# Performance work log

Measured on AMD Instinct MI355X. Metric: run time of the kernel, lower is better.

## Reference

```python
import jax, jax.numpy as jnp
import numpy as np

B, C, H, W = 32, 32, 64, 64   # batch, in_channel, image height/width
HC = 1                        # hashtable channel groups (in_channel % HC == 0)
KS = 9                        # kernel_size: top-k neighbors per pixel
K = 64                        # kernel_number_per_pixel (output channels)
P = H * W                     # pixel_number


def setup_inputs() -> dict:
    key = jax.random.key(0)
    k1, k2, k3 = jax.random.split(key, 3)
    x = jax.random.normal(k1, (B, C, H, W), dtype=jnp.float32)
    # Per-pixel affinity scores -> top-KS neighbor indices (mimics
    # _build_full_hash: argsort descending, take first kernel_size).
    scores = jax.random.normal(k2, (HC, H, W, P), dtype=jnp.float32)
    idx = jnp.argsort(-scores, axis=-1)[..., :KS].astype(jnp.int32)  # (HC, NH, NW, KS)
    bound = float(np.sqrt(1.0 / (C * KS)))
    weights = jax.random.uniform(k3, (K, C * KS), minval=-bound, maxval=bound,
                                 dtype=jnp.float32)
    return {"x": x, "weights": weights, "idx": idx}


def reference(x, weights, idx):
    Bx, Cx, Hx, Wx = x.shape
    HCx, NH, NW, ks = idx.shape
    Px = Hx * Wx
    # full_hash[b, c, i, j, k] = idx[c % HC, i, j, k] + c*P + b*C*P,
    # so x.take(full_hash) == gather of x[b, c] at idx[c % HC].
    idx_full = jnp.tile(idx, (Cx // HCx, 1, 1, 1)).reshape(Cx, NH * NW * ks)
    g = jnp.take_along_axis(x.reshape(Bx, Cx, Px), idx_full[None], axis=2)  # (B, C, NH*NW*ks)
    # permute(1,4,0,2,3).reshape(C*ks, B*NH*NW)
    g = g.reshape(Bx, Cx, NH, NW, ks).transpose(1, 4, 0, 2, 3).reshape(Cx * ks, Bx * NH * NW)
    out = (weights @ g).reshape(-1, Bx, NH, NW)  # (K, B, NH, NW)
    return jnp.transpose(out, (1, 0, 2, 3))       # (B, K, NH, NW)
```

## Files before the change

### kernel.cpp

```cpp
#include <hip/hip_runtime.h>
#include <hip/hip_bf16.h>

#define BB 32
#define CC 32
#define PP 4096
#define KS 9
#define KK 64
#define CK 288

typedef __attribute__((ext_vector_type(8))) short short8;
typedef __attribute__((ext_vector_type(16))) float f32x16;

__device__ inline unsigned short f2bf(float f) {
    __hip_bfloat16 h = __float2bfloat16(f);
    return __builtin_bit_cast(unsigned short, h);
}

__global__ __launch_bounds__(256)
void prep_kernel(const float* __restrict__ x, const float* __restrict__ w,
                 unsigned short* __restrict__ xt, unsigned short* __restrict__ wa) {
    const int t = threadIdx.x;
    const int blk = blockIdx.x;
    if (blk < 512) {
        const int b = blk >> 4;
        const int p = ((blk & 15) << 8) + t;
        const float* xb = x + (size_t)b * CC * PP + p;
        unsigned int buf[16];
#pragma unroll
        for (int c2 = 0; c2 < 16; ++c2) {
            float lo = xb[(size_t)(2 * c2) * PP];
            float hi = xb[(size_t)(2 * c2 + 1) * PP];
            buf[c2] = (unsigned int)f2bf(lo) | ((unsigned int)f2bf(hi) << 16);
        }
        uint4* dst = (uint4*)(xt + ((size_t)b * PP + p) * CC);
        const uint4* s = (const uint4*)buf;
#pragma unroll
        for (int j = 0; j < 4; ++j) dst[j] = s[j];
    } else {
        int i = (blk - 512) * 256 + t;
        if (i < KK * CK) {
            int j  = i & 7;
            int l  = (i >> 3) & 63;
            int mt = (i >> 9) & 1;
            int kh = (i >> 10) & 1;
            int kc = i >> 11;
            int ko = (mt << 5) + (l & 31);
            int c  = (kh << 4) + ((l >> 5) << 3) + j;
            wa[i] = f2bf(w[ko * CK + c * KS + kc]);
        }
    }
}

__global__ __launch_bounds__(256, 4)
void abc_mfma5_kernel(const unsigned short* __restrict__ xt,
                      const unsigned short* __restrict__ wa,
                      const int* __restrict__ idx,
                      float* __restrict__ out) {
    __shared__ unsigned short was[KK * CK];
    const int t    = threadIdx.x;
    const int l    = t & 63;
    const int w    = t >> 6;
    const int blk  = blockIdx.x;
    const int b    = ((blk & 7) << 2) | ((blk >> 3) & 3);
    const int tile = blk >> 5;
    const int p0   = (tile << 7) + (w << 5);
    const int gpix  = l & 31;
    const int ghalf = l >> 5;

    {
        const uint4* s = (const uint4*)wa;
        uint4* d = (uint4*)was;
#pragma unroll
        for (int j = 0; j < 9; ++j) d[t + 256 * j] = s[t + 256 * j];
    }

    const unsigned short* xtb = xt + (size_t)b * PP * CC;

    int q[KS];
    {
        const int* ip = idx + (size_t)(p0 + gpix) * KS;
#pragma unroll
        for (int kc = 0; kc < KS; ++kc) q[kc] = ip[kc];
    }

    f32x16 acc[2];
#pragma unroll
    for (int i = 0; i < 16; ++i) { acc[0][i] = 0.f; acc[1][i] = 0.f; }

    __syncthreads();

    short8 g[3][2];
#pragma unroll
    for (int kk = 0; kk < 2; ++kk)
#pragma unroll
        for (int kh = 0; kh < 2; ++kh)
            g[kk][kh] = *(const short8*)(xtb + (size_t)q[kk] * CC + (kh << 4) + (ghalf << 3));

#pragma unroll
    for (int kc = 0; kc < KS; ++kc) {
        if (kc + 2 < KS) {
            const int nb = (kc + 2) % 3;
#pragma unroll
            for (int kh = 0; kh < 2; ++kh)
                g[nb][kh] = *(const short8*)(xtb + (size_t)q[kc + 2] * CC + (kh << 4) + (ghalf << 3));
        }
        const int cb = kc % 3;
#pragma unroll
        for (int mt = 0; mt < 2; ++mt) {
#pragma unroll
            for (int kh = 0; kh < 2; ++kh) {
                const short8 a =
                    *(const short8*)(was + ((size_t)(((kc * 2 + kh) * 2 + mt) * 64 + l)) * 8);
                acc[mt] = __builtin_amdgcn_mfma_f32_32x32x16_bf16(a, g[cb][kh], acc[mt], 0, 0, 0);
            }
        }
    }

    float* ob = out + (size_t)b * KK * PP + p0 + gpix;
#pragma unroll
    for (int mt = 0; mt < 2; ++mt)
#pragma unroll
        for (int r = 0; r < 16; ++r) {
            const int row = (mt << 5) + (r & 3) + ((r >> 2) << 3) + (ghalf << 2);
            __builtin_nontemporal_store(acc[mt][r], ob + (size_t)row * PP);
        }
}

__global__ __launch_bounds__(256)
void abc_valu_kernel(const float* __restrict__ x, const float* __restrict__ w,
                     const int* __restrict__ idx, float* __restrict__ out) {
    __shared__ float xrow[PP];
    const int t = threadIdx.x;
    const int b = blockIdx.x >> 4;
    const int p = ((blockIdx.x & 15) << 8) + t;
    int q[KS];
#pragma unroll
    for (int k = 0; k < KS; ++k) q[k] = idx[p * KS + k];
    float acc[KK];
#pragma unroll
    for (int i = 0; i < KK; ++i) acc[i] = 0.0f;
    const float* xb = x + (size_t)b * CC * PP;
#pragma unroll 1
    for (int c = 0; c < CC; ++c) {
        const float4* src = (const float4*)(xb + (size_t)c * PP);
        float4* dst = (float4*)xrow;
#pragma unroll
        for (int j = 0; j < 4; ++j) dst[j * 256 + t] = src[j * 256 + t];
        __syncthreads();
        float xv[KS];
#pragma unroll
        for (int k = 0; k < KS; ++k) xv[k] = xrow[q[k]];
#pragma unroll
        for (int k = 0; k < KS; ++k) {
            const int col = c * KS + k;
#pragma unroll
            for (int ko = 0; ko < KK; ++ko)
                acc[ko] += xv[k] * w[ko * CK + col];
        }
        __syncthreads();
    }
    float* ob = out + (size_t)b * KK * PP + p;
#pragma unroll
    for (int ko = 0; ko < KK; ++ko)
        ob[(size_t)ko * PP] = acc[ko];
}

extern "C" void kernel_launch(void* const* d_in, const int* in_sizes, int n_in,
                              void* d_out, int out_size, void* d_ws, size_t ws_size,
                              hipStream_t stream) {
    const float* x  = (const float*)d_in[0];
    const float* w  = (const float*)d_in[1];
    const int* idx  = (const int*)d_in[2];
    float* out      = (float*)d_out;

    const size_t xt_bytes = (size_t)BB * PP * CC * 2;
    const size_t need     = xt_bytes + (size_t)KK * CK * 2;

    if (ws_size >= need) {
        unsigned short* xt = (unsigned short*)d_ws;
        unsigned short* wa = (unsigned short*)((char*)d_ws + xt_bytes);
        const int wb_blocks = (KK * CK + 255) / 256;
        prep_kernel<<<512 + wb_blocks, 256, 0, stream>>>(x, w, xt, wa);
        abc_mfma5_kernel<<<BB * (PP / 128), 256, 0, stream>>>(xt, wa, idx, out);
    } else {
        abc_valu_kernel<<<BB * (PP / 256), 256, 0, stream>>>(x, w, idx, out);
    }
}
```

Before: 88.57 us.

## Fuse bf16 conversion and gather-GEMM into one kernel with LDS-resident image

Replaces the two-kernel pipeline (prep into a channel-last bf16 workspace, then MFMA gather) with one 1024-thread kernel. Each block stages half the channels of a whole image as packed bf16 in LDS, builds the weight fragments in LDS, and gathers neighbors from LDS instead of global memory. This removes the workspace round trip and one launch. In exchange each image is read and weights re-converted by 8 blocks, the grid drops to 256 large blocks with a big LDS footprint (about 150 KB), and the fallback VALU path is removed.

Result: no change. 86.98 us (-1.8%).

```diff
diff --git a/kernel.cpp b/kernel.cpp
--- a/kernel.cpp
+++ b/kernel.cpp
@@ -9,6 +9,7 @@
 #define CK 288
 
 typedef __attribute__((ext_vector_type(8))) short short8;
+typedef __attribute__((ext_vector_type(4))) int int4v;
 typedef __attribute__((ext_vector_type(16))) float f32x16;
 
 __device__ inline unsigned short f2bf(float f) {
@@ -16,65 +17,21 @@
     return __builtin_bit_cast(unsigned short, h);
 }
 
-__global__ __launch_bounds__(256)
-void prep_kernel(const float* __restrict__ x, const float* __restrict__ w,
-                 unsigned short* __restrict__ xt, unsigned short* __restrict__ wa) {
-    const int t = threadIdx.x;
-    const int blk = blockIdx.x;
-    if (blk < 512) {
-        const int b = blk >> 4;
-        const int p = ((blk & 15) << 8) + t;
-        const float* xb = x + (size_t)b * CC * PP + p;
-        unsigned int buf[16];
-#pragma unroll
-        for (int c2 = 0; c2 < 16; ++c2) {
-            float lo = xb[(size_t)(2 * c2) * PP];
-            float hi = xb[(size_t)(2 * c2 + 1) * PP];
-            buf[c2] = (unsigned int)f2bf(lo) | ((unsigned int)f2bf(hi) << 16);
-        }
-        uint4* dst = (uint4*)(xt + ((size_t)b * PP + p) * CC);
-        const uint4* s = (const uint4*)buf;
-#pragma unroll
-        for (int j = 0; j < 4; ++j) dst[j] = s[j];
-    } else {
-        int i = (blk - 512) * 256 + t;
-        if (i < KK * CK) {
-            int j  = i & 7;
-            int l  = (i >> 3) & 63;
-            int mt = (i >> 9) & 1;
-            int kh = (i >> 10) & 1;
-            int kc = i >> 11;
-            int ko = (mt << 5) + (l & 31);
-            int c  = (kh << 4) + ((l >> 5) << 3) + j;
-            wa[i] = f2bf(w[ko * CK + c * KS + kc]);
-        }
-    }
-}
+__global__ __launch_bounds__(1024)
+void abc_fused_kernel(const float* __restrict__ x, const float* __restrict__ w,
+                      const int* __restrict__ idx, float* __restrict__ out) {
+    __shared__ unsigned int   xs4[8 * 4100];
+    __shared__ unsigned short wah[9 * 2 * 64 * 8];
 
-__global__ __launch_bounds__(256, 4)
-void abc_mfma5_kernel(const unsigned short* __restrict__ xt,
-                      const unsigned short* __restrict__ wa,
-                      const int* __restrict__ idx,
-                      float* __restrict__ out) {
-    __shared__ unsigned short was[KK * CK];
-    const int t    = threadIdx.x;
-    const int l    = t & 63;
-    const int w    = t >> 6;
-    const int blk  = blockIdx.x;
-    const int b    = ((blk & 7) << 2) | ((blk >> 3) & 3);
-    const int tile = blk >> 5;
-    const int p0   = (tile << 7) + (w << 5);
+    const int t     = threadIdx.x;
+    const int l     = t & 63;
+    const int wv    = t >> 6;
+    const int blk   = blockIdx.x;
+    const int b     = ((blk & 7) << 2) | ((blk >> 3) & 3);
+    const int pb    = blk >> 5;
+    const int p0    = pb * 512 + wv * 32;
     const int gpix  = l & 31;
     const int ghalf = l >> 5;
-
-    {
-        const uint4* s = (const uint4*)wa;
-        uint4* d = (uint4*)was;
-#pragma unroll
-        for (int j = 0; j < 9; ++j) d[t + 256 * j] = s[t + 256 * j];
-    }
-
-    const unsigned short* xtb = xt + (size_t)b * PP * CC;
 
     int q[KS];
     {
@@ -87,31 +44,50 @@
 #pragma unroll
     for (int i = 0; i < 16; ++i) { acc[0][i] = 0.f; acc[1][i] = 0.f; }
 
-    __syncthreads();
-
-    short8 g[3][2];
-#pragma unroll
-    for (int kk = 0; kk < 2; ++kk)
-#pragma unroll
-        for (int kh = 0; kh < 2; ++kh)
-            g[kk][kh] = *(const short8*)(xtb + (size_t)q[kk] * CC + (kh << 4) + (ghalf << 3));
+    const float* xb0 = x + (size_t)b * CC * PP;
 
 #pragma unroll
-    for (int kc = 0; kc < KS; ++kc) {
-        if (kc + 2 < KS) {
-            const int nb = (kc + 2) % 3;
+    for (int half = 0; half < 2; ++half) {
+        if (half) __syncthreads();
+
+        const float* xh = xb0 + (size_t)(half * 16) * PP;
 #pragma unroll
-            for (int kh = 0; kh < 2; ++kh)
-                g[nb][kh] = *(const short8*)(xtb + (size_t)q[kc + 2] * CC + (kh << 4) + (ghalf << 3));
+        for (int c2 = 0; c2 < 8; ++c2) {
+            const float4 lo = *(const float4*)(xh + (size_t)(2 * c2) * PP + 4 * t);
+            const float4 hi = *(const float4*)(xh + (size_t)(2 * c2 + 1) * PP + 4 * t);
+            uint4 v;
+            v.x = (unsigned)f2bf(lo.x) | ((unsigned)f2bf(hi.x) << 16);
+            v.y = (unsigned)f2bf(lo.y) | ((unsigned)f2bf(hi.y) << 16);
+            v.z = (unsigned)f2bf(lo.z) | ((unsigned)f2bf(hi.z) << 16);
+            v.w = (unsigned)f2bf(lo.w) | ((unsigned)f2bf(hi.w) << 16);
+            *(uint4*)(&xs4[c2 * 4100 + 4 * t]) = v;
         }
-        const int cb = kc % 3;
+
 #pragma unroll
-        for (int mt = 0; mt < 2; ++mt) {
+        for (int i = 0; i < 9; ++i) {
+            const int wi = t + (i << 10);
+            const int j  = wi & 7;
+            const int ll = (wi >> 3) & 63;
+            const int mt = (wi >> 9) & 1;
+            const int kc = wi >> 10;
+            const int ko = (mt << 5) + (ll & 31);
+            const int c  = (half << 4) + ((ll >> 5) << 3) + j;
+            wah[wi] = f2bf(w[ko * CK + c * KS + kc]);
+        }
+
+        __syncthreads();
+
 #pragma unroll
-            for (int kh = 0; kh < 2; ++kh) {
-                const short8 a =
-                    *(const short8*)(was + ((size_t)(((kc * 2 + kh) * 2 + mt) * 64 + l)) * 8);
-                acc[mt] = __builtin_amdgcn_mfma_f32_32x32x16_bf16(a, g[cb][kh], acc[mt], 0, 0, 0);
+        for (int kc = 0; kc < KS; ++kc) {
+            int4v r;
+#pragma unroll
+            for (int jj = 0; jj < 4; ++jj)
+                r[jj] = (int)xs4[(ghalf * 4 + jj) * 4100 + q[kc]];
+            const short8 bf = __builtin_bit_cast(short8, r);
+#pragma unroll
+            for (int mt = 0; mt < 2; ++mt) {
+                const short8 a = *(const short8*)&wah[(((kc << 1) + mt) * 64 + l) * 8];
+                acc[mt] = __builtin_amdgcn_mfma_f32_32x32x16_bf16(a, bf, acc[mt], 0, 0, 0);
             }
         }
     }
@@ -126,45 +102,6 @@
         }
 }
 
-__global__ __launch_bounds__(256)
-void abc_valu_kernel(const float* __restrict__ x, const float* __restrict__ w,
-                     const int* __restrict__ idx, float* __restrict__ out) {
-    __shared__ float xrow[PP];
-    const int t = threadIdx.x;
-    const int b = blockIdx.x >> 4;
-    const int p = ((blockIdx.x & 15) << 8) + t;
-    int q[KS];
-#pragma unroll
-    for (int k = 0; k < KS; ++k) q[k] = idx[p * KS + k];
-    float acc[KK];
-#pragma unroll
-    for (int i = 0; i < KK; ++i) acc[i] = 0.0f;
-    const float* xb = x + (size_t)b * CC * PP;
-#pragma unroll 1
-    for (int c = 0; c < CC; ++c) {
-        const float4* src = (const float4*)(xb + (size_t)c * PP);
-        float4* dst = (float4*)xrow;
-#pragma unroll
-        for (int j = 0; j < 4; ++j) dst[j * 256 + t] = src[j * 256 + t];
-        __syncthreads();
-        float xv[KS];
-#pragma unroll
-        for (int k = 0; k < KS; ++k) xv[k] = xrow[q[k]];
-#pragma unroll
-        for (int k = 0; k < KS; ++k) {
-            const int col = c * KS + k;
-#pragma unroll
-            for (int ko = 0; ko < KK; ++ko)
-                acc[ko] += xv[k] * w[ko * CK + col];
-        }
-        __syncthreads();
-    }
-    float* ob = out + (size_t)b * KK * PP + p;
-#pragma unroll
-    for (int ko = 0; ko < KK; ++ko)
-        ob[(size_t)ko * PP] = acc[ko];
-}
-
 extern "C" void kernel_launch(void* const* d_in, const int* in_sizes, int n_in,
                               void* d_out, int out_size, void* d_ws, size_t ws_size,
                               hipStream_t stream) {
@@ -172,17 +109,7 @@
     const float* w  = (const float*)d_in[1];
     const int* idx  = (const int*)d_in[2];
     float* out      = (float*)d_out;
+    (void)d_ws; (void)ws_size;
 
-    const size_t xt_bytes = (size_t)BB * PP * CC * 2;
-    const size_t need     = xt_bytes + (size_t)KK * CK * 2;
-
-    if (ws_size >= need) {
-        unsigned short* xt = (unsigned short*)d_ws;
-        unsigned short* wa = (unsigned short*)((char*)d_ws + xt_bytes);
-        const int wb_blocks = (KK * CK + 255) / 256;
-        prep_kernel<<<512 + wb_blocks, 256, 0, stream>>>(x, w, xt, wa);
-        abc_mfma5_kernel<<<BB * (PP / 128), 256, 0, stream>>>(xt, wa, idx, out);
-    } else {
-        abc_valu_kernel<<<BB * (PP / 256), 256, 0, stream>>>(x, w, idx, out);
-    }
+    abc_fused_kernel<<<256, 1024, 0, stream>>>(x, w, idx, out);
 }
```

## Fuse bf16 conversion of x into MFMA kernel with LDS-staged channel groups

Applied to the files above, without the earlier changes.

Drops the separate prep pass that wrote a transposed bf16 copy of x to global memory. Each 1024-thread block now loads 8 channels of one image at a time, converts them to bf16 and stages them in double-buffered padded LDS. The neighbor gather then comes from LDS instead of scattered global reads. Weights are streamed per channel group in a new 4-wide packing, and the loads for the next group are prefetched while the MFMAs run. The cost is only 256 blocks with large LDS use (low occupancy), two barriers per group, and each block re-reading x for its pixel range.

New measurement: 92.49 us. 4.4% more time.

```diff
diff --git a/kernel.cpp b/kernel.cpp
--- a/kernel.cpp
+++ b/kernel.cpp
@@ -7,74 +7,51 @@
 #define KS 9
 #define KK 64
 #define CK 288
+#define PADP 4100
 
 typedef __attribute__((ext_vector_type(8))) short short8;
+typedef __attribute__((ext_vector_type(4))) float f32x4;
+typedef __attribute__((ext_vector_type(4))) int int4v;
+typedef __attribute__((ext_vector_type(2))) unsigned int u32x2;
+typedef __attribute__((ext_vector_type(4))) unsigned int u32x4;
 typedef __attribute__((ext_vector_type(16))) float f32x16;
 
-__device__ inline unsigned short f2bf(float f) {
+__device__ inline unsigned int f2bf(float f) {
     __hip_bfloat16 h = __float2bfloat16(f);
-    return __builtin_bit_cast(unsigned short, h);
+    return (unsigned int)__builtin_bit_cast(unsigned short, h);
 }
 
 __global__ __launch_bounds__(256)
-void prep_kernel(const float* __restrict__ x, const float* __restrict__ w,
-                 unsigned short* __restrict__ xt, unsigned short* __restrict__ wa) {
-    const int t = threadIdx.x;
-    const int blk = blockIdx.x;
-    if (blk < 512) {
-        const int b = blk >> 4;
-        const int p = ((blk & 15) << 8) + t;
-        const float* xb = x + (size_t)b * CC * PP + p;
-        unsigned int buf[16];
-#pragma unroll
-        for (int c2 = 0; c2 < 16; ++c2) {
-            float lo = xb[(size_t)(2 * c2) * PP];
-            float hi = xb[(size_t)(2 * c2 + 1) * PP];
-            buf[c2] = (unsigned int)f2bf(lo) | ((unsigned int)f2bf(hi) << 16);
-        }
-        uint4* dst = (uint4*)(xt + ((size_t)b * PP + p) * CC);
-        const uint4* s = (const uint4*)buf;
-#pragma unroll
-        for (int j = 0; j < 4; ++j) dst[j] = s[j];
-    } else {
-        int i = (blk - 512) * 256 + t;
-        if (i < KK * CK) {
-            int j  = i & 7;
-            int l  = (i >> 3) & 63;
-            int mt = (i >> 9) & 1;
-            int kh = (i >> 10) & 1;
-            int kc = i >> 11;
-            int ko = (mt << 5) + (l & 31);
-            int c  = (kh << 4) + ((l >> 5) << 3) + j;
-            wa[i] = f2bf(w[ko * CK + c * KS + kc]);
-        }
-    }
+void prep_wa4_kernel(const float* __restrict__ w, unsigned short* __restrict__ wa4) {
+    const int i = blockIdx.x * 256 + threadIdx.x;
+    if (i >= KK * CK) return;
+    const int j    = i & 3;
+    const int l    = (i >> 2) & 63;
+    const int mt   = (i >> 8) & 1;
+    const int rest = i >> 9;
+    const int qq   = rest / 9;
+    const int kc   = rest - qq * 9;
+    const int ko   = (mt << 5) + (l & 31);
+    const int c    = (qq << 3) + (((l >> 5) & 1) << 2) + j;
+    wa4[i] = (unsigned short)f2bf(w[ko * CK + c * KS + kc]);
 }
 
-__global__ __launch_bounds__(256, 4)
-void abc_mfma5_kernel(const unsigned short* __restrict__ xt,
-                      const unsigned short* __restrict__ wa,
-                      const int* __restrict__ idx,
-                      float* __restrict__ out) {
-    __shared__ unsigned short was[KK * CK];
+__global__ __launch_bounds__(1024)
+void abc_fused8_kernel(const float* __restrict__ x,
+                       const unsigned short* __restrict__ wa4,
+                       const int* __restrict__ idx,
+                       float* __restrict__ out) {
+    __shared__ unsigned long long xq[2][2 * PADP];
+    __shared__ unsigned int wsl[2304];
     const int t    = threadIdx.x;
     const int l    = t & 63;
-    const int w    = t >> 6;
+    const int wv   = t >> 6;
     const int blk  = blockIdx.x;
     const int b    = ((blk & 7) << 2) | ((blk >> 3) & 3);
-    const int tile = blk >> 5;
-    const int p0   = (tile << 7) + (w << 5);
-    const int gpix  = l & 31;
-    const int ghalf = l >> 5;
-
-    {
-        const uint4* s = (const uint4*)wa;
-        uint4* d = (uint4*)was;
-#pragma unroll
-        for (int j = 0; j < 9; ++j) d[t + 256 * j] = s[t + 256 * j];
-    }
-
-    const unsigned short* xtb = xt + (size_t)b * PP * CC;
+    const int pb   = blk >> 5;
+    const int p0   = pb * 512 + wv * 32;
+    const int gpix = l & 31;
+    const int gh   = l >> 5;
 
     int q[KS];
     {
@@ -83,37 +60,65 @@
         for (int kc = 0; kc < KS; ++kc) q[kc] = ip[kc];
     }
 
+    const float* xb = x + (size_t)b * CC * PP;
+    const unsigned int* wag = (const unsigned int*)wa4;
+
     f32x16 acc[2];
 #pragma unroll
     for (int i = 0; i < 16; ++i) { acc[0][i] = 0.f; acc[1][i] = 0.f; }
 
-    __syncthreads();
+    f32x4 xr[8];
+#pragma unroll
+    for (int ch = 0; ch < 8; ++ch)
+        xr[ch] = *(const f32x4*)(xb + (size_t)ch * PP + 4 * t);
+    unsigned int wr0 = wag[t];
+    unsigned int wr1 = wag[1024 + t];
+    unsigned int wr2 = 0;
+    if (t < 256) wr2 = wag[2048 + t];
 
-    short8 g[3][2];
+#pragma unroll 1
+    for (int qq = 0; qq < 4; ++qq) {
 #pragma unroll
-    for (int kk = 0; kk < 2; ++kk)
+        for (int g2 = 0; g2 < 2; ++g2) {
+            unsigned int lo[4], hi[4];
 #pragma unroll
-        for (int kh = 0; kh < 2; ++kh)
-            g[kk][kh] = *(const short8*)(xtb + (size_t)q[kk] * CC + (kh << 4) + (ghalf << 3));
+            for (int jp = 0; jp < 4; ++jp) {
+                lo[jp] = f2bf(xr[4 * g2 + 0][jp]) | (f2bf(xr[4 * g2 + 1][jp]) << 16);
+                hi[jp] = f2bf(xr[4 * g2 + 2][jp]) | (f2bf(xr[4 * g2 + 3][jp]) << 16);
+            }
+            u32x4* d = (u32x4*)&xq[qq & 1][(size_t)g2 * PADP + 4 * t];
+            d[0] = (u32x4){lo[0], hi[0], lo[1], hi[1]};
+            d[1] = (u32x4){lo[2], hi[2], lo[3], hi[3]};
+        }
+        wsl[t] = wr0;
+        wsl[1024 + t] = wr1;
+        if (t < 256) wsl[2048 + t] = wr2;
+        __syncthreads();
+
+        if (qq < 3) {
+#pragma unroll
+            for (int ch = 0; ch < 8; ++ch)
+                xr[ch] = *(const f32x4*)(xb + (size_t)((qq + 1) * 8 + ch) * PP + 4 * t);
+            const int base = (qq + 1) * 2304;
+            wr0 = wag[base + t];
+            wr1 = wag[base + 1024 + t];
+            if (t < 256) wr2 = wag[base + 2048 + t];
+        }
 
 #pragma unroll
-    for (int kc = 0; kc < KS; ++kc) {
-        if (kc + 2 < KS) {
-            const int nb = (kc + 2) % 3;
+        for (int kc = 0; kc < KS; ++kc) {
+            const u32x2 bg = *(const u32x2*)&xq[qq & 1][(size_t)gh * PADP + q[kc]];
+            const int4v bi = {(int)bg[0], (int)bg[1], 0, 0};
+            const short8 b8 = __builtin_bit_cast(short8, bi);
 #pragma unroll
-            for (int kh = 0; kh < 2; ++kh)
-                g[nb][kh] = *(const short8*)(xtb + (size_t)q[kc + 2] * CC + (kh << 4) + (ghalf << 3));
-        }
-        const int cb = kc % 3;
-#pragma unroll
-        for (int mt = 0; mt < 2; ++mt) {
-#pragma unroll
-            for (int kh = 0; kh < 2; ++kh) {
-                const short8 a =
-                    *(const short8*)(was + ((size_t)(((kc * 2 + kh) * 2 + mt) * 64 + l)) * 8);
-                acc[mt] = __builtin_amdgcn_mfma_f32_32x32x16_bf16(a, g[cb][kh], acc[mt], 0, 0, 0);
+            for (int mt = 0; mt < 2; ++mt) {
+                const u32x2 ag = *(const u32x2*)&wsl[((kc * 2 + mt) * 64 + l) * 2];
+                const int4v ai = {(int)ag[0], (int)ag[1], 0, 0};
+                const short8 a8 = __builtin_bit_cast(short8, ai);
+                acc[mt] = __builtin_amdgcn_mfma_f32_32x32x16_bf16(a8, b8, acc[mt], 0, 0, 0);
             }
         }
+        __syncthreads();
     }
 
     float* ob = out + (size_t)b * KK * PP + p0 + gpix;
@@ -121,7 +126,7 @@
     for (int mt = 0; mt < 2; ++mt)
 #pragma unroll
         for (int r = 0; r < 16; ++r) {
-            const int row = (mt << 5) + (r & 3) + ((r >> 2) << 3) + (ghalf << 2);
+            const int row = (mt << 5) + (r & 3) + ((r >> 2) << 3) + (gh << 2);
             __builtin_nontemporal_store(acc[mt][r], ob + (size_t)row * PP);
         }
 }
@@ -173,15 +178,12 @@
     const int* idx  = (const int*)d_in[2];
     float* out      = (float*)d_out;
 
-    const size_t xt_bytes = (size_t)BB * PP * CC * 2;
-    const size_t need     = xt_bytes + (size_t)KK * CK * 2;
+    const size_t need = (size_t)KK * CK * 2;
 
     if (ws_size >= need) {
-        unsigned short* xt = (unsigned short*)d_ws;
-        unsigned short* wa = (unsigned short*)((char*)d_ws + xt_bytes);
-        const int wb_blocks = (KK * CK + 255) / 256;
-        prep_kernel<<<512 + wb_blocks, 256, 0, stream>>>(x, w, xt, wa);
-        abc_mfma5_kernel<<<BB * (PP / 128), 256, 0, stream>>>(xt, wa, idx, out);
+        unsigned short* wa4 = (unsigned short*)d_ws;
+        prep_wa4_kernel<<<(KK * CK + 255) / 256, 256, 0, stream>>>(w, wa4);
+        abc_fused8_kernel<<<256, 1024, 0, stream>>>(x, wa4, idx, out);
     } else {
         abc_valu_kernel<<<BB * (PP / 256), 256, 0, stream>>>(x, w, idx, out);
     }
```
